# Kernel optimization log

Hardware: AMD Instinct MI355X
Metric: run time of the kernel (lower is better)

The kernel has to match this reference:

```python
import jax, jax.numpy as jnp
import numpy as np

S, B, D_MODEL, H, DH = 2048, 2, 1024, 16, 64
FACTOR = 1.0 / np.sqrt(DH).astype(np.float32)


def setup_inputs() -> dict:
    key = jax.random.key(0)
    ks = jax.random.split(key, 12)
    sc = 0.02
    inp = {
        'query': jax.random.normal(ks[0], (S, B, D_MODEL), jnp.float32),
        'key': jax.random.normal(ks[1], (S, B, D_MODEL), jnp.float32),
        'value': jax.random.normal(ks[2], (S, B, D_MODEL), jnp.float32),
        # causal mask [seq_q, seq_k, 1]; 0 -> masked
        'mask': jnp.tril(jnp.ones((S, S), dtype=bool))[:, :, None],
        'Wq': jax.random.normal(ks[3], (H * DH, D_MODEL), jnp.float32) * sc,
        'bq': jnp.zeros((H * DH,), jnp.float32),
        'Wk': jax.random.normal(ks[4], (H * DH, D_MODEL), jnp.float32) * sc,
        'bk': jnp.zeros((H * DH,), jnp.float32),
        'Wv': jax.random.normal(ks[5], (H * DH, D_MODEL), jnp.float32) * sc,
        'bv': jnp.zeros((H * DH,), jnp.float32),
        'Wo': jax.random.normal(ks[6], (D_MODEL, H * DH), jnp.float32) * sc,
        'bo': jnp.zeros((D_MODEL,), jnp.float32),
    }
    return inp


def _split_heads(x):
    # pattern: 's b (head_dim head_num) -> s b head_num head_dim' (head_dim is OUTER)
    s, b, _ = x.shape
    return x.reshape(s, b, DH, H).transpose(0, 1, 3, 2)  # [s,b,H,DH]


def reference(query, key, value, mask, Wq, bq, Wk, bk, Wv, bv, Wo, bo):
    q = _split_heads(query @ Wq.T + bq)
    k = _split_heads(key @ Wk.T + bk)
    v = _split_heads(value @ Wv.T + bv)
    scores = jnp.einsum('ibhd,jbhd->ijbh', q, k) * FACTOR  # [i,j,b,h]
    scores = jnp.where(mask[..., None], scores, -jnp.inf)
    attn = jax.nn.softmax(scores, axis=1)  # softmax over keys (dim=1)
    out = jnp.einsum('ijbh,jbhd->ibhd', attn, v)  # [i,b,h,d]
    out = out.reshape(S, B, H * DH)  # 'i b h d -> i b (h d)'
    return out @ Wo.T + bo
```

## Files before the change

kernel.cpp:

```cpp
#include <hip/hip_runtime.h>


typedef float f32x4 __attribute__((ext_vector_type(4)));
typedef float f32x16 __attribute__((ext_vector_type(16)));
typedef __bf16 bf16x8_t __attribute__((ext_vector_type(8)));
typedef unsigned short ushort8 __attribute__((ext_vector_type(8)));
typedef unsigned int uint4v __attribute__((ext_vector_type(4)));
typedef unsigned int uint2v __attribute__((ext_vector_type(2)));

#define S_LEN 2048
#define BATCH 2
#define DMODEL 1024
#define NHEAD 16
#define DHEAD 64
#define K_SCALE 0.18033688011112042f

__device__ __forceinline__ unsigned short f2bf(float x) {
  unsigned int u = __builtin_bit_cast(unsigned int, x);
  u += 0x7fffu + ((u >> 16) & 1u);
  return (unsigned short)(u >> 16);
}

__device__ __forceinline__ f32x4 mfma16(ushort8 a, ushort8 b, f32x4 c) {
  return __builtin_amdgcn_mfma_f32_16x16x32_bf16(
      __builtin_bit_cast(bf16x8_t, a), __builtin_bit_cast(bf16x8_t, b), c, 0, 0, 0);
}
__device__ __forceinline__ f32x16 mfma32(ushort8 a, ushort8 b, f32x16 c) {
  return __builtin_amdgcn_mfma_f32_32x32x16_bf16(
      __builtin_bit_cast(bf16x8_t, a), __builtin_bit_cast(bf16x8_t, b), c, 0, 0, 0);
}

__device__ __forceinline__ float max3f(float a, float b, float c) {
  return fmaxf(fmaxf(a, b), c);
}

__device__ __forceinline__ ushort8 pack8(float4 a, float4 b, float s) {
  ushort8 t;
  t[0] = f2bf(a.x * s); t[1] = f2bf(a.y * s); t[2] = f2bf(a.z * s); t[3] = f2bf(a.w * s);
  t[4] = f2bf(b.x * s); t[5] = f2bf(b.y * s); t[6] = f2bf(b.z * s); t[7] = f2bf(b.w * s);
  return t;
}

__device__ __forceinline__ void gload16(unsigned short* lds, const unsigned short* g) {
  __builtin_amdgcn_global_load_lds(
      (const __attribute__((address_space(1))) unsigned int*)g,
      (__attribute__((address_space(3))) unsigned int*)lds, 16, 0, 0);
}

__global__ __launch_bounds__(256) void cvt_kernel(
    const float* __restrict__ q, const float* __restrict__ k, const float* __restrict__ v,
    const float* __restrict__ wq, const float* __restrict__ wk,
    const float* __restrict__ wv, const float* __restrict__ wo,
    unsigned short* __restrict__ qB, unsigned short* __restrict__ kB,
    unsigned short* __restrict__ vB, unsigned short* __restrict__ wqB,
    unsigned short* __restrict__ wkB, unsigned short* __restrict__ wvB,
    unsigned short* __restrict__ woB)
{
  const int c = blockIdx.x * 256 + threadIdx.x;
  const float* s; unsigned short* d; int base;
  if      (c < 524288)  { s = q;  d = qB;  base = 0; }
  else if (c < 1048576) { s = k;  d = kB;  base = 524288; }
  else if (c < 1572864) { s = v;  d = vB;  base = 1048576; }
  else if (c < 1703936) { s = wq; d = wqB; base = 1572864; }
  else if (c < 1835008) { s = wk; d = wkB; base = 1703936; }
  else if (c < 1966080) { s = wv; d = wvB; base = 1835008; }
  else                  { s = wo; d = woB; base = 1966080; }
  const size_t off = (size_t)(c - base) * 8;
  const float4 v0 = *reinterpret_cast<const float4*>(s + off);
  const float4 v1 = *reinterpret_cast<const float4*>(s + off + 4);
  *reinterpret_cast<ushort8*>(d + off) = pack8(v0, v1, 1.0f);
}

__global__ __launch_bounds__(256) void gemm_qkv_kernel(
    const unsigned short* __restrict__ qA, const unsigned short* __restrict__ kA,
    const unsigned short* __restrict__ vA,
    const unsigned short* __restrict__ wqW, const unsigned short* __restrict__ wkW,
    const unsigned short* __restrict__ wvW,
    const float* __restrict__ bq, const float* __restrict__ bk,
    const float* __restrict__ bv,
    unsigned short* __restrict__ Cq, unsigned short* __restrict__ Ck,
    unsigned short* __restrict__ Cv)
{
  __shared__ __align__(16) unsigned short As[2][128 * 64];
  __shared__ __align__(16) unsigned short Ws[2][64 * 64];
  const int z = blockIdx.z;
  const unsigned short* A = (z == 0) ? qA : (z == 1) ? kA : vA;
  const unsigned short* W = (z == 0) ? wqW : (z == 1) ? wkW : wvW;
  const float* bias = (z == 0) ? bq : (z == 1) ? bk : bv;
  unsigned short* C = (z == 0) ? Cq : (z == 1) ? Ck : Cv;
  const float oscale = (z == 1) ? K_SCALE : 1.0f;

  const int tid = threadIdx.x;
  const int lane = tid & 63;
  const int w = tid >> 6;
  const int wm = (w >> 1) * 64, wn = (w & 1) * 32;
  const int g = lane >> 4, lr = lane & 15;

  const int bid = (int)blockIdx.x;
  const int widx = (bid & 7) * 64 + (bid >> 3);
  const int n0 = (widx & 15) * 64;
  const int m0 = (widx >> 4) * 128;

  f32x4 acc[4][2] = {};

#define STAGE(buf, k0)                                                              \
  {                                                                                 \
    _Pragma("unroll")                                                               \
    for (int ii = 0; ii < 4; ++ii) {                                                \
      const int c = ii * 256 + tid;                                                 \
      const int row = c >> 3;                                                       \
      const int sl = (c & 7) ^ (row & 7);                                           \
      gload16(&As[buf][c * 8], A + (size_t)(m0 + row) * DMODEL + (k0) + sl * 8);    \
    }                                                                               \
    _Pragma("unroll")                                                               \
    for (int ii = 0; ii < 2; ++ii) {                                                \
      const int c = ii * 256 + tid;                                                 \
      const int row = c >> 3;                                                       \
      const int sl = (c & 7) ^ (row & 7);                                           \
      gload16(&Ws[buf][c * 8], W + (size_t)(n0 + row) * DMODEL + (k0) + sl * 8);    \
    }                                                                               \
  }

  STAGE(0, 0);
  int cur = 0;

  for (int t = 0; t < 16; ++t) {
    __syncthreads();
    if (t < 15) STAGE(cur ^ 1, (t + 1) * 64);

    const char* ab = (const char*)&As[cur][0];
    const char* wb = (const char*)&Ws[cur][0];
#pragma unroll
    for (int kk = 0; kk < 2; ++kk) {
      ushort8 af[4], bw[2];
#pragma unroll
      for (int mt = 0; mt < 4; ++mt) {
        const int row = wm + mt * 16 + lr;
        af[mt] = *reinterpret_cast<const ushort8*>(
            ab + row * 128 + (((kk * 4 + g) ^ (row & 7)) << 4));
      }
#pragma unroll
      for (int nt = 0; nt < 2; ++nt) {
        const int row = wn + nt * 16 + lr;
        bw[nt] = *reinterpret_cast<const ushort8*>(
            wb + row * 128 + (((kk * 4 + g) ^ (row & 7)) << 4));
      }
      __builtin_amdgcn_s_setprio(1);
#pragma unroll
      for (int mt = 0; mt < 4; ++mt)
#pragma unroll
        for (int nt = 0; nt < 2; ++nt)
          acc[mt][nt] = mfma16(af[mt], bw[nt], acc[mt][nt]);
      __builtin_amdgcn_s_setprio(0);
    }
    cur ^= 1;
  }
#undef STAGE

#pragma unroll
  for (int nt = 0; nt < 2; ++nt) {
    const int col = n0 + wn + nt * 16 + lr;
    const float bvv = bias[col];
#pragma unroll
    for (int mt = 0; mt < 4; ++mt)
#pragma unroll
      for (int r = 0; r < 4; ++r) {
        const int rowg = m0 + wm + mt * 16 + g * 4 + r;
        C[(size_t)rowg * DMODEL + col] = f2bf((acc[mt][nt][r] + bvv) * oscale);
      }
  }
}

__global__ __launch_bounds__(256) void gemm_out_kernel(
    const unsigned short* __restrict__ A, const unsigned short* __restrict__ W,
    const float* __restrict__ bias, float* __restrict__ C)
{
  __shared__ __align__(16) unsigned short As[2][128 * 64];
  __shared__ __align__(16) unsigned short Ws[2][64 * 64];
  const int tid = threadIdx.x;
  const int lane = tid & 63;
  const int w = tid >> 6;
  const int wm = (w >> 1) * 64, wn = (w & 1) * 32;
  const int g = lane >> 4, lr = lane & 15;

  const int bid = (int)blockIdx.x;
  const int widx = (bid & 7) * 64 + (bid >> 3);
  const int n0 = (widx & 15) * 64;
  const int m0 = (widx >> 4) * 128;

  f32x4 acc[4][2] = {};

#define STAGE(buf, k0)                                                              \
  {                                                                                 \
    _Pragma("unroll")                                                               \
    for (int ii = 0; ii < 4; ++ii) {                                                \
      const int c = ii * 256 + tid;                                                 \
      const int row = c >> 3;                                                       \
      const int sl = (c & 7) ^ (row & 7);                                           \
      gload16(&As[buf][c * 8], A + (size_t)(m0 + row) * DMODEL + (k0) + sl * 8);    \
    }                                                                               \
    _Pragma("unroll")                                                               \
    for (int ii = 0; ii < 2; ++ii) {                                                \
      const int c = ii * 256 + tid;                                                 \
      const int row = c >> 3;                                                       \
      const int sl = (c & 7) ^ (row & 7);                                           \
      gload16(&Ws[buf][c * 8], W + (size_t)(n0 + row) * DMODEL + (k0) + sl * 8);    \
    }                                                                               \
  }

  STAGE(0, 0);
  int cur = 0;

  for (int t = 0; t < 16; ++t) {
    __syncthreads();
    if (t < 15) STAGE(cur ^ 1, (t + 1) * 64);

    const char* ab = (const char*)&As[cur][0];
    const char* wb = (const char*)&Ws[cur][0];
#pragma unroll
    for (int kk = 0; kk < 2; ++kk) {
      ushort8 af[4], bw[2];
#pragma unroll
      for (int mt = 0; mt < 4; ++mt) {
        const int row = wm + mt * 16 + lr;
        af[mt] = *reinterpret_cast<const ushort8*>(
            ab + row * 128 + (((kk * 4 + g) ^ (row & 7)) << 4));
      }
#pragma unroll
      for (int nt = 0; nt < 2; ++nt) {
        const int row = wn + nt * 16 + lr;
        bw[nt] = *reinterpret_cast<const ushort8*>(
            wb + row * 128 + (((kk * 4 + g) ^ (row & 7)) << 4));
      }
      __builtin_amdgcn_s_setprio(1);
#pragma unroll
      for (int mt = 0; mt < 4; ++mt)
#pragma unroll
        for (int nt = 0; nt < 2; ++nt)
          acc[mt][nt] = mfma16(af[mt], bw[nt], acc[mt][nt]);
      __builtin_amdgcn_s_setprio(0);
    }
    cur ^= 1;
  }
#undef STAGE

#pragma unroll
  for (int nt = 0; nt < 2; ++nt) {
    const int col = n0 + wn + nt * 16 + lr;
    const float bvv = bias[col];
#pragma unroll
    for (int mt = 0; mt < 4; ++mt)
#pragma unroll
      for (int r = 0; r < 4; ++r) {
        const int rowg = m0 + wm + mt * 16 + g * 4 + r;
        C[(size_t)rowg * DMODEL + col] = acc[mt][nt][r] + bvv;
      }
  }
}

__global__ __launch_bounds__(256) void head_tr0_kernel(
    const unsigned short* __restrict__ in0, unsigned short* __restrict__ out0,
    const unsigned short* __restrict__ in1, unsigned short* __restrict__ out1)
{
  const unsigned short* in = blockIdx.z ? in1 : in0;
  unsigned short* out = blockIdx.z ? out1 : out0;
  __shared__ __align__(16) unsigned short T[32 * 256];
  const int tid = threadIdx.x;
  const int n0 = blockIdx.x * 32, o0 = blockIdx.y * 256;
#pragma unroll
  for (int i = 0; i < 4; ++i) {
    const int c = i * 256 + tid;
    const int row = c >> 5, c8 = c & 31;
    ushort8 v = *reinterpret_cast<const ushort8*>(in + (size_t)(n0 + row) * DMODEL + o0 + c8 * 8);
    int y = (row * 512 + c8 * 16) ^ ((row & 3) << 5);
    *reinterpret_cast<ushort8*>((char*)T + y) = v;
  }
  __syncthreads();
  const int d0 = o0 >> 4, s0 = n0 >> 1;
#pragma unroll
  for (int rep = 0; rep < 2; ++rep) {
    const int e = rep * 256 + tid;
    const int hh = e & 15, s = (e >> 4) & 15, b = (e >> 8) & 1;
    const int n = s * 2 + b;
    unsigned short vals[16];
#pragma unroll
    for (int dd = 0; dd < 16; ++dd) {
      int y = n * 512 + ((dd * 32 + hh * 2) ^ ((n & 3) << 5));
      vals[dd] = *(const unsigned short*)((const char*)T + y);
    }
    uint4v w0, w1;
#pragma unroll
    for (int j = 0; j < 4; ++j) {
      w0[j] = (unsigned)vals[2 * j] | ((unsigned)vals[2 * j + 1] << 16);
      w1[j] = (unsigned)vals[8 + 2 * j] | ((unsigned)vals[8 + 2 * j + 1] << 16);
    }
    unsigned short* dst = out + ((size_t)(b * 16 + hh) * S_LEN + s0 + s) * DHEAD + d0;
    *reinterpret_cast<uint4v*>(dst) = w0;
    *reinterpret_cast<uint4v*>(dst + 8) = w1;
  }
}

__global__ __launch_bounds__(256) void head_tr1_kernel(
    const unsigned short* __restrict__ in, unsigned short* __restrict__ out)
{
  __shared__ __align__(16) unsigned short T[64 * 64];
  const int tid = threadIdx.x;
  const int n0 = blockIdx.x * 64, o0 = blockIdx.y * 64;
#pragma unroll
  for (int i = 0; i < 2; ++i) {
    const int c = i * 256 + tid;
    const int row = c >> 3, c8 = c & 7;
    ushort8 v = *reinterpret_cast<const ushort8*>(in + (size_t)(n0 + row) * DMODEL + o0 + c8 * 8);
    int y = (row * 128 + c8 * 16) ^ ((row & 7) << 4);
    *reinterpret_cast<ushort8*>((char*)T + y) = v;
  }
  __syncthreads();
  const int d0 = o0 >> 4, s0 = n0 >> 1;
  const int shalf = tid & 1, seg = tid >> 1;
  const int dd = seg & 3, hh = (seg >> 2) & 15, b = (seg >> 6) & 1;
  unsigned short vals[16];
#pragma unroll
  for (int i = 0; i < 16; ++i) {
    const int s = shalf * 16 + i;
    const int n = s * 2 + b;
    int y = n * 128 + (((dd * 16 + hh) * 2) ^ ((n & 7) << 4));
    vals[i] = *(const unsigned short*)((const char*)T + y);
  }
  uint4v w0, w1;
#pragma unroll
  for (int j = 0; j < 4; ++j) {
    w0[j] = (unsigned)vals[2 * j] | ((unsigned)vals[2 * j + 1] << 16);
    w1[j] = (unsigned)vals[8 + 2 * j] | ((unsigned)vals[8 + 2 * j + 1] << 16);
  }
  unsigned short* dst = out + ((size_t)(b * 16 + hh) * DHEAD + d0 + dd) * S_LEN + s0 + shalf * 16;
  *reinterpret_cast<uint4v*>(dst) = w0;
  *reinterpret_cast<uint4v*>(dst + 8) = w1;
}

__global__ __launch_bounds__(256, 4) void attn_part_kernel(
    const unsigned short* __restrict__ Qh, const unsigned short* __restrict__ Kh,
    const unsigned short* __restrict__ Vh, unsigned short* __restrict__ Opart,
    float* __restrict__ mlbuf)
{
  __shared__ __align__(16) unsigned short Ks[2][64 * 64];
  __shared__ __align__(16) unsigned short Vs[2][64 * 64];

  const int tid = threadIdx.x;
  const int lane = tid & 63;
  const int w = tid >> 6;
  const int ln31 = lane & 31;
  const int hf = lane >> 5;

  const int u = 39 - (int)blockIdx.x;
  int Q, c;
  if      (u < 4)  { Q = u;                 c = 0; }
  else if (u < 12) { Q = 4 + ((u - 4) >> 1);  c = (u - 4) & 1; }
  else if (u < 24) { Q = 8 + (u - 12) / 3;    c = (u - 12) % 3; }
  else             { Q = 12 + ((u - 24) >> 2); c = (u - 24) & 3; }
  int off;
  if      (Q < 4)  off = Q;
  else if (Q < 8)  off = 4 + (Q - 4) * 2;
  else if (Q < 12) off = 12 + (Q - 8) * 3;
  else             off = 24 + (Q - 12) * 4;

  const int hb = blockIdx.y;
  const int head = hb & 15, b = hb >> 4;
  const int slot = hb * 40 + off + c;
  const int t0 = c * 8;
  const int tmax = 2 * Q + 1;
  const int t1 = (tmax < t0 + 7) ? tmax : (t0 + 7);
  const int q0 = Q * 128;

  const size_t hoff = (size_t)(b * NHEAD + head) * (S_LEN * DHEAD);
  const unsigned short* Qg = Qh + hoff;
  const unsigned short* Kg = Kh + hoff;
  const unsigned short* Vg = Vh + hoff;

  const int qwb = q0 + w * 32;
  const int qg = qwb + ln31;

  ushort8 qf[4];
#pragma unroll
  for (int kt = 0; kt < 4; ++kt)
    qf[kt] = *reinterpret_cast<const ushort8*>(Qg + (size_t)qg * DHEAD + kt * 16 + hf * 8);

  f32x16 oa0 = {0}, oa1 = {0};
  float mrun = -1e30f, ssum = 0.f;

#define STAGE(buf, kv)                                                             \
  {                                                                                \
    _Pragma("unroll")                                                              \
    for (int ii = 0; ii < 2; ++ii) {                                               \
      const int c2 = ii * 256 + tid;                                               \
      const int row = c2 >> 3;                                                     \
      const int sl = (c2 & 7) ^ (row & 7);                                         \
      gload16(&Ks[buf][c2 * 8], Kg + (size_t)((kv) + row) * 64 + sl * 8);          \
    }                                                                              \
    _Pragma("unroll")                                                              \
    for (int ii = 0; ii < 2; ++ii) {                                               \
      const int c2 = ii * 256 + tid;                                               \
      const int row = c2 >> 3;                                                     \
      const int sl = (c2 & 7) ^ (row & 7);                                         \
      gload16(&Vs[buf][c2 * 8], Vg + (size_t)row * S_LEN + (kv) + sl * 8);         \
    }                                                                              \
  }

  STAGE(0, t0 * 64);
  int cur = 0;

  const int kb0 = ln31 * 128 + ((hf * 16) ^ ((ln31 & 7) << 4));
  const int kb1 = (32 + ln31) * 128 + ((hf * 16) ^ ((ln31 & 7) << 4));

  for (int t = t0; t <= t1; ++t) {
    const int kv0 = t * 64;
    __syncthreads();
    if (t < t1) STAGE(cur ^ 1, kv0 + 64);

    if (kv0 <= qwb + 31) {
      f32x16 sc0 = {0}, sc1 = {0};
      {
        const char* ksb = (const char*)&Ks[cur][0];
        __builtin_amdgcn_s_setprio(1);
#pragma unroll
        for (int kt = 0; kt < 4; ++kt) {
          ushort8 kf0 = *reinterpret_cast<const ushort8*>(ksb + (kb0 ^ (kt << 5)));
          ushort8 kf1 = *reinterpret_cast<const ushort8*>(ksb + (kb1 ^ (kt << 5)));
          sc0 = mfma32(kf0, qf[kt], sc0);
          sc1 = mfma32(kf1, qf[kt], sc1);
        }
        __builtin_amdgcn_s_setprio(0);
      }

      if (kv0 + 63 > qwb) {
#pragma unroll
        for (int r = 0; r < 16; ++r) {
          const int keyb = kv0 + (r & 3) + 8 * (r >> 2) + 4 * hf;
          if (keyb > qg) sc0[r] = -1e30f;
          if (keyb + 32 > qg) sc1[r] = -1e30f;
        }
      }

      float m0a = max3f(sc0[0], sc0[1], sc0[2]);
      float m1a = max3f(sc0[3], sc0[4], sc0[5]);
      float m2a = max3f(sc0[6], sc0[7], sc0[8]);
      float m3a = max3f(sc0[9], sc0[10], sc0[11]);
      float m4a = max3f(sc0[12], sc0[13], sc0[14]);
      float m5a = max3f(sc0[15], sc1[0], sc1[1]);
      float m6a = max3f(sc1[2], sc1[3], sc1[4]);
      float m7a = max3f(sc1[5], sc1[6], sc1[7]);
      float m8a = max3f(sc1[8], sc1[9], sc1[10]);
      float m9a = max3f(sc1[11], sc1[12], sc1[13]);
      float mAa = fmaxf(sc1[14], sc1[15]);
      float n0a = max3f(m0a, m1a, m2a);
      float n1a = max3f(m3a, m4a, m5a);
      float n2a = max3f(m6a, m7a, m8a);
      float n3a = fmaxf(m9a, mAa);
      float pmax = fmaxf(max3f(n0a, n1a, n2a), n3a);
      pmax = fmaxf(pmax, __shfl_xor(pmax, 32, 64));

      if (!__all(pmax <= mrun + 8.0f)) {
        const float mnew = fmaxf(mrun, pmax);
        const float scl = exp2f(mrun - mnew);
        ssum *= scl;
#pragma unroll
        for (int r = 0; r < 16; ++r) { oa0[r] *= scl; oa1[r] *= scl; }
        mrun = mnew;
      }

      float pv0[16], pv1[16];
#pragma unroll
      for (int r = 0; r < 16; ++r) {
        pv0[r] = exp2f(sc0[r] - mrun);
        pv1[r] = exp2f(sc1[r] - mrun);
      }
      float a8[8];
#pragma unroll
      for (int r = 0; r < 8; ++r)
        a8[r] = (pv0[r] + pv0[r + 8]) + (pv1[r] + pv1[r + 8]);
      float a4_0 = a8[0] + a8[4], a4_1 = a8[1] + a8[5];
      float a4_2 = a8[2] + a8[6], a4_3 = a8[3] + a8[7];
      float psum = (a4_0 + a4_1) + (a4_2 + a4_3);
      psum += __shfl_xor(psum, 32, 64);
      ssum += psum;

      unsigned int cc[16], pc[16];
#pragma unroll
      for (int j = 0; j < 8; ++j) {
        asm("v_cvt_pk_bf16_f32 %0, %1, %2" : "=v"(cc[j]) : "v"(pv0[2 * j]), "v"(pv0[2 * j + 1]));
        asm("v_cvt_pk_bf16_f32 %0, %1, %2" : "=v"(cc[8 + j]) : "v"(pv1[2 * j]), "v"(pv1[2 * j + 1]));
      }
#pragma unroll
      for (int j = 0; j < 16; ++j)
        pc[j] = (unsigned int)__shfl_xor((int)cc[j], 32, 64);

      uint4v pfw[4];
#pragma unroll
      for (int mt = 0; mt < 2; ++mt) {
#pragma unroll
        for (int ktl = 0; ktl < 2; ++ktl) {
          const int o = mt * 8 + ktl * 4;
          uint4v u4;
          u4[0] = hf ? pc[o + 2] : cc[o + 0];
          u4[1] = hf ? pc[o + 3] : cc[o + 1];
          u4[2] = hf ? cc[o + 2] : pc[o + 0];
          u4[3] = hf ? cc[o + 3] : pc[o + 1];
          pfw[mt * 2 + ktl] = u4;
        }
      }

      {
        const char* vsb = (const char*)&Vs[cur][0];
        __builtin_amdgcn_s_setprio(1);
#pragma unroll
        for (int kt = 0; kt < 4; ++kt) {
          ushort8 vf0 = *reinterpret_cast<const ushort8*>(vsb + (kb0 ^ (kt << 5)));
          ushort8 vf1 = *reinterpret_cast<const ushort8*>(vsb + (kb1 ^ (kt << 5)));
          ushort8 pfr = __builtin_bit_cast(ushort8, pfw[kt]);
          oa0 = mfma32(vf0, pfr, oa0);
          oa1 = mfma32(vf1, pfr, oa1);
        }
        __builtin_amdgcn_s_setprio(0);
      }
    }

    cur ^= 1;
  }
#undef STAGE

  const int ql = w * 32 + ln31;
  unsigned short* ob = Opart + (size_t)slot * 8192 + ql * 64;
#pragma unroll
  for (int mt2 = 0; mt2 < 2; ++mt2) {
#pragma unroll
    for (int rq = 0; rq < 4; ++rq) {
      const int dd = mt2 * 32 + 8 * rq + 4 * hf;
      const f32x16& a = mt2 ? oa1 : oa0;
      unsigned int w0, w1;
      asm("v_cvt_pk_bf16_f32 %0, %1, %2" : "=v"(w0)
          : "v"(a[4 * rq + 0]), "v"(a[4 * rq + 1]));
      asm("v_cvt_pk_bf16_f32 %0, %1, %2" : "=v"(w1)
          : "v"(a[4 * rq + 2]), "v"(a[4 * rq + 3]));
      uint2v pk = { w0, w1 };
      *reinterpret_cast<uint2v*>(ob + dd) = pk;
    }
  }
  if (hf == 0) {
    mlbuf[slot * 256 + ql] = mrun;
    mlbuf[slot * 256 + 128 + ql] = ssum;
  }
}

__global__ __launch_bounds__(256) void attn_combine_kernel(
    const unsigned short* __restrict__ Opart, const float* __restrict__ mlbuf,
    unsigned short* __restrict__ O)
{
  const int Q = blockIdx.x, hb = blockIdx.y;
  const int head = hb & 15, b = hb >> 4;
  const int nch = (2 * Q + 1) / 8 + 1;
  int off;
  if      (Q < 4)  off = Q;
  else if (Q < 8)  off = 4 + (Q - 4) * 2;
  else if (Q < 12) off = 12 + (Q - 8) * 3;
  else             off = 24 + (Q - 12) * 4;
  const int s0 = hb * 40 + off;

  const int tid = threadIdx.x;
  const int q = tid >> 1, dh = (tid & 1) * 32;

  float mc[4], lc[4];
  float M = -1e30f;
  for (int cc = 0; cc < nch; ++cc) {
    mc[cc] = mlbuf[(s0 + cc) * 256 + q];
    lc[cc] = mlbuf[(s0 + cc) * 256 + 128 + q];
    M = fmaxf(M, mc[cc]);
  }
  float L = 0.f, wgt[4];
  for (int cc = 0; cc < nch; ++cc) {
    wgt[cc] = exp2f(mc[cc] - M);
    L += wgt[cc] * lc[cc];
  }
  const float invL = 1.0f / L;

  float acc[32] = {};
  for (int cc = 0; cc < nch; ++cc) {
    const unsigned short* p = Opart + (size_t)(s0 + cc) * 8192 + q * 64 + dh;
    const float wv = wgt[cc];
#pragma unroll
    for (int seg = 0; seg < 4; ++seg) {
      ushort8 v = *reinterpret_cast<const ushort8*>(p + seg * 8);
#pragma unroll
      for (int j = 0; j < 8; ++j) {
        const float f = __builtin_bit_cast(float, ((unsigned int)v[j]) << 16);
        acc[seg * 8 + j] += wv * f;
      }
    }
  }

  unsigned int wpk[16];
#pragma unroll
  for (int j = 0; j < 16; ++j) {
    asm("v_cvt_pk_bf16_f32 %0, %1, %2" : "=v"(wpk[j])
        : "v"(acc[2 * j] * invL), "v"(acc[2 * j + 1] * invL));
  }
  unsigned short* dst = O + ((size_t)((Q * 128 + q) * BATCH + b)) * DMODEL + head * DHEAD + dh;
#pragma unroll
  for (int seg = 0; seg < 4; ++seg)
    *reinterpret_cast<uint4v*>(dst + seg * 8) =
        uint4v{ wpk[4 * seg], wpk[4 * seg + 1], wpk[4 * seg + 2], wpk[4 * seg + 3] };
}

extern "C" void kernel_launch(void* const* d_in, const int* in_sizes, int n_in,
                              void* d_out, int out_size, void* d_ws, size_t ws_size,
                              hipStream_t stream)
{
  (void)in_sizes; (void)n_in; (void)out_size; (void)ws_size;
  const float* query = (const float*)d_in[0];
  const float* key_  = (const float*)d_in[1];
  const float* value = (const float*)d_in[2];
  const float* Wq = (const float*)d_in[4];
  const float* bq = (const float*)d_in[5];
  const float* Wk = (const float*)d_in[6];
  const float* bk = (const float*)d_in[7];
  const float* Wv = (const float*)d_in[8];
  const float* bv = (const float*)d_in[9];
  const float* Wo = (const float*)d_in[10];
  const float* bo = (const float*)d_in[11];
  float* out = (float*)d_out;

  const size_t NE = (size_t)4096 * DMODEL;
  const size_t NW = (size_t)DMODEL * DMODEL;
  unsigned short* qB  = (unsigned short*)d_ws;
  unsigned short* kB  = qB + NE;
  unsigned short* vB  = kB + NE;
  unsigned short* g1  = vB + NE;
  unsigned short* Qh  = g1 + NE;
  unsigned short* Kh  = Qh + NE;
  unsigned short* Vh  = Kh + NE;
  unsigned short* wqB = Vh + NE;
  unsigned short* wkB = wqB + NW;
  unsigned short* wvB = wkB + NW;
  unsigned short* woB = wvB + NW;
  unsigned short* Opart = vB;
  float* mlbuf = (float*)(vB + (size_t)1280 * 8192);

  cvt_kernel<<<dim3(8192), 256, 0, stream>>>(query, key_, value, Wq, Wk, Wv, Wo,
                                             qB, kB, vB, wqB, wkB, wvB, woB);
  gemm_qkv_kernel<<<dim3(512, 1, 3), 256, 0, stream>>>(
      qB, kB, vB, wqB, wkB, wvB, bq, bk, bv, g1, Qh, Kh);
  head_tr0_kernel<<<dim3(128, 4, 2), 256, 0, stream>>>(g1, qB, Qh, Vh);
  head_tr1_kernel<<<dim3(64, 16), 256, 0, stream>>>(Kh, kB);
  attn_part_kernel<<<dim3(40, 32), 256, 0, stream>>>(qB, Vh, kB, Opart, mlbuf);
  attn_combine_kernel<<<dim3(16, 32), 256, 0, stream>>>(Opart, mlbuf, qB);
  gemm_out_kernel<<<dim3(512), 256, 0, stream>>>(qB, woB, bo, out);
}
```

Measured before the change: 141.3 us.

## Merge head transposes into one launch and rebalance attention chunks to six tiles

Combines the two head-transpose kernels into a single launch that dispatches on block index, removing one kernel launch and its tail. The split-KV attention now uses chunks of up to six key tiles (51 chunks per head-batch instead of 40), with a loop-based mapping from block to (query tile, chunk). The combine kernel is adjusted to handle up to six partial chunks. The goal is better load balance and more blocks to fill the GPU, at the cost of more partial outputs to write and merge, and a change in block scheduling order (the old code processed the heaviest query tiles first).

```diff
diff --git a/kernel.cpp b/kernel.cpp
--- a/kernel.cpp
+++ b/kernel.cpp
@@ -14,6 +14,7 @@
 #define NHEAD 16
 #define DHEAD 64
 #define K_SCALE 0.18033688011112042f
+#define NCHUNK 51
 
 __device__ __forceinline__ unsigned short f2bf(float x) {
   unsigned int u = __builtin_bit_cast(unsigned int, x);
@@ -258,35 +259,73 @@
   }
 }
 
-__global__ __launch_bounds__(256) void head_tr0_kernel(
+__global__ __launch_bounds__(256) void transpose_all_kernel(
     const unsigned short* __restrict__ in0, unsigned short* __restrict__ out0,
-    const unsigned short* __restrict__ in1, unsigned short* __restrict__ out1)
+    const unsigned short* __restrict__ in1, unsigned short* __restrict__ out1,
+    const unsigned short* __restrict__ in2, unsigned short* __restrict__ out2)
 {
-  const unsigned short* in = blockIdx.z ? in1 : in0;
-  unsigned short* out = blockIdx.z ? out1 : out0;
   __shared__ __align__(16) unsigned short T[32 * 256];
+  const int bx = (int)blockIdx.x;
   const int tid = threadIdx.x;
-  const int n0 = blockIdx.x * 32, o0 = blockIdx.y * 256;
-#pragma unroll
-  for (int i = 0; i < 4; ++i) {
-    const int c = i * 256 + tid;
-    const int row = c >> 5, c8 = c & 31;
-    ushort8 v = *reinterpret_cast<const ushort8*>(in + (size_t)(n0 + row) * DMODEL + o0 + c8 * 8);
-    int y = (row * 512 + c8 * 16) ^ ((row & 3) << 5);
-    *reinterpret_cast<ushort8*>((char*)T + y) = v;
-  }
-  __syncthreads();
-  const int d0 = o0 >> 4, s0 = n0 >> 1;
-#pragma unroll
-  for (int rep = 0; rep < 2; ++rep) {
-    const int e = rep * 256 + tid;
-    const int hh = e & 15, s = (e >> 4) & 15, b = (e >> 8) & 1;
-    const int n = s * 2 + b;
+
+  if (bx < 1024) {
+    const unsigned short* in = (bx < 512) ? in0 : in1;
+    unsigned short* out = (bx < 512) ? out0 : out1;
+    const int lb = bx & 511;
+    const int n0 = (lb & 127) * 32, o0 = (lb >> 7) * 256;
+#pragma unroll
+    for (int i = 0; i < 4; ++i) {
+      const int c = i * 256 + tid;
+      const int row = c >> 5, c8 = c & 31;
+      ushort8 v = *reinterpret_cast<const ushort8*>(in + (size_t)(n0 + row) * DMODEL + o0 + c8 * 8);
+      int y = (row * 512 + c8 * 16) ^ ((row & 3) << 5);
+      *reinterpret_cast<ushort8*>((char*)T + y) = v;
+    }
+    __syncthreads();
+    const int d0 = o0 >> 4, s0 = n0 >> 1;
+#pragma unroll
+    for (int rep = 0; rep < 2; ++rep) {
+      const int e = rep * 256 + tid;
+      const int hh = e & 15, s = (e >> 4) & 15, b = (e >> 8) & 1;
+      const int n = s * 2 + b;
+      unsigned short vals[16];
+#pragma unroll
+      for (int dd = 0; dd < 16; ++dd) {
+        int y = n * 512 + ((dd * 32 + hh * 2) ^ ((n & 3) << 5));
+        vals[dd] = *(const unsigned short*)((const char*)T + y);
+      }
+      uint4v w0, w1;
+#pragma unroll
+      for (int j = 0; j < 4; ++j) {
+        w0[j] = (unsigned)vals[2 * j] | ((unsigned)vals[2 * j + 1] << 16);
+        w1[j] = (unsigned)vals[8 + 2 * j] | ((unsigned)vals[8 + 2 * j + 1] << 16);
+      }
+      unsigned short* dst = out + ((size_t)(b * 16 + hh) * S_LEN + s0 + s) * DHEAD + d0;
+      *reinterpret_cast<uint4v*>(dst) = w0;
+      *reinterpret_cast<uint4v*>(dst + 8) = w1;
+    }
+  } else {
+    const int lb = bx - 1024;
+    const int n0 = (lb & 63) * 64, o0 = (lb >> 6) * 64;
+#pragma unroll
+    for (int i = 0; i < 2; ++i) {
+      const int c = i * 256 + tid;
+      const int row = c >> 3, c8 = c & 7;
+      ushort8 v = *reinterpret_cast<const ushort8*>(in2 + (size_t)(n0 + row) * DMODEL + o0 + c8 * 8);
+      int y = (row * 128 + c8 * 16) ^ ((row & 7) << 4);
+      *reinterpret_cast<ushort8*>((char*)T + y) = v;
+    }
+    __syncthreads();
+    const int d0 = o0 >> 4, s0 = n0 >> 1;
+    const int shalf = tid & 1, seg = tid >> 1;
+    const int dd = seg & 3, hh = (seg >> 2) & 15, b = (seg >> 6) & 1;
     unsigned short vals[16];
 #pragma unroll
-    for (int dd = 0; dd < 16; ++dd) {
-      int y = n * 512 + ((dd * 32 + hh * 2) ^ ((n & 3) << 5));
-      vals[dd] = *(const unsigned short*)((const char*)T + y);
+    for (int i = 0; i < 16; ++i) {
+      const int s = shalf * 16 + i;
+      const int n = s * 2 + b;
+      int y = n * 128 + (((dd * 16 + hh) * 2) ^ ((n & 7) << 4));
+      vals[i] = *(const unsigned short*)((const char*)T + y);
     }
     uint4v w0, w1;
 #pragma unroll
@@ -294,47 +333,10 @@
       w0[j] = (unsigned)vals[2 * j] | ((unsigned)vals[2 * j + 1] << 16);
       w1[j] = (unsigned)vals[8 + 2 * j] | ((unsigned)vals[8 + 2 * j + 1] << 16);
     }
-    unsigned short* dst = out + ((size_t)(b * 16 + hh) * S_LEN + s0 + s) * DHEAD + d0;
+    unsigned short* dst = out2 + ((size_t)(b * 16 + hh) * DHEAD + d0 + dd) * S_LEN + s0 + shalf * 16;
     *reinterpret_cast<uint4v*>(dst) = w0;
     *reinterpret_cast<uint4v*>(dst + 8) = w1;
   }
-}
-
-__global__ __launch_bounds__(256) void head_tr1_kernel(
-    const unsigned short* __restrict__ in, unsigned short* __restrict__ out)
-{
-  __shared__ __align__(16) unsigned short T[64 * 64];
-  const int tid = threadIdx.x;
-  const int n0 = blockIdx.x * 64, o0 = blockIdx.y * 64;
-#pragma unroll
-  for (int i = 0; i < 2; ++i) {
-    const int c = i * 256 + tid;
-    const int row = c >> 3, c8 = c & 7;
-    ushort8 v = *reinterpret_cast<const ushort8*>(in + (size_t)(n0 + row) * DMODEL + o0 + c8 * 8);
-    int y = (row * 128 + c8 * 16) ^ ((row & 7) << 4);
-    *reinterpret_cast<ushort8*>((char*)T + y) = v;
-  }
-  __syncthreads();
-  const int d0 = o0 >> 4, s0 = n0 >> 1;
-  const int shalf = tid & 1, seg = tid >> 1;
-  const int dd = seg & 3, hh = (seg >> 2) & 15, b = (seg >> 6) & 1;
-  unsigned short vals[16];
-#pragma unroll
-  for (int i = 0; i < 16; ++i) {
-    const int s = shalf * 16 + i;
-    const int n = s * 2 + b;
-    int y = n * 128 + (((dd * 16 + hh) * 2) ^ ((n & 7) << 4));
-    vals[i] = *(const unsigned short*)((const char*)T + y);
-  }
-  uint4v w0, w1;
-#pragma unroll
-  for (int j = 0; j < 4; ++j) {
-    w0[j] = (unsigned)vals[2 * j] | ((unsigned)vals[2 * j + 1] << 16);
-    w1[j] = (unsigned)vals[8 + 2 * j] | ((unsigned)vals[8 + 2 * j + 1] << 16);
-  }
-  unsigned short* dst = out + ((size_t)(b * 16 + hh) * DHEAD + d0 + dd) * S_LEN + s0 + shalf * 16;
-  *reinterpret_cast<uint4v*>(dst) = w0;
-  *reinterpret_cast<uint4v*>(dst + 8) = w1;
 }
 
 __global__ __launch_bounds__(256, 4) void attn_part_kernel(
@@ -351,24 +353,17 @@
   const int ln31 = lane & 31;
   const int hf = lane >> 5;
 
-  const int u = 39 - (int)blockIdx.x;
-  int Q, c;
-  if      (u < 4)  { Q = u;                 c = 0; }
-  else if (u < 12) { Q = 4 + ((u - 4) >> 1);  c = (u - 4) & 1; }
-  else if (u < 24) { Q = 8 + (u - 12) / 3;    c = (u - 12) % 3; }
-  else             { Q = 12 + ((u - 24) >> 2); c = (u - 24) & 3; }
-  int off;
-  if      (Q < 4)  off = Q;
-  else if (Q < 8)  off = 4 + (Q - 4) * 2;
-  else if (Q < 12) off = 12 + (Q - 8) * 3;
-  else             off = 24 + (Q - 12) * 4;
+  int u = (int)blockIdx.x;
+  int Q = 0, nc = 1;
+  while (u >= nc) { u -= nc; ++Q; nc = Q / 3 + 1; }
+  const int c = u;
 
   const int hb = blockIdx.y;
   const int head = hb & 15, b = hb >> 4;
-  const int slot = hb * 40 + off + c;
-  const int t0 = c * 8;
+  const int slot = hb * NCHUNK + (int)blockIdx.x;
+  const int t0 = c * 6;
   const int tmax = 2 * Q + 1;
-  const int t1 = (tmax < t0 + 7) ? tmax : (t0 + 7);
+  const int t1 = (tmax < t0 + 5) ? tmax : (t0 + 5);
   const int q0 = Q * 128;
 
   const size_t hoff = (size_t)(b * NHEAD + head) * (S_LEN * DHEAD);
@@ -556,25 +551,22 @@
 {
   const int Q = blockIdx.x, hb = blockIdx.y;
   const int head = hb & 15, b = hb >> 4;
-  const int nch = (2 * Q + 1) / 8 + 1;
-  int off;
-  if      (Q < 4)  off = Q;
-  else if (Q < 8)  off = 4 + (Q - 4) * 2;
-  else if (Q < 12) off = 12 + (Q - 8) * 3;
-  else             off = 24 + (Q - 12) * 4;
-  const int s0 = hb * 40 + off;
+  const int nch = Q / 3 + 1;
+  int off = 0;
+  for (int j = 0; j < Q; ++j) off += j / 3 + 1;
+  const int s0 = hb * NCHUNK + off;
 
   const int tid = threadIdx.x;
   const int q = tid >> 1, dh = (tid & 1) * 32;
 
-  float mc[4], lc[4];
+  float mc[6], lc[6];
   float M = -1e30f;
   for (int cc = 0; cc < nch; ++cc) {
     mc[cc] = mlbuf[(s0 + cc) * 256 + q];
     lc[cc] = mlbuf[(s0 + cc) * 256 + 128 + q];
     M = fmaxf(M, mc[cc]);
   }
-  float L = 0.f, wgt[4];
+  float L = 0.f, wgt[6];
   for (int cc = 0; cc < nch; ++cc) {
     wgt[cc] = exp2f(mc[cc] - M);
     L += wgt[cc] * lc[cc];
@@ -641,15 +633,14 @@
   unsigned short* wvB = wkB + NW;
   unsigned short* woB = wvB + NW;
   unsigned short* Opart = vB;
-  float* mlbuf = (float*)(vB + (size_t)1280 * 8192);
+  float* mlbuf = (float*)(Opart + (size_t)(NCHUNK * 32) * 8192);
 
   cvt_kernel<<<dim3(8192), 256, 0, stream>>>(query, key_, value, Wq, Wk, Wv, Wo,
                                              qB, kB, vB, wqB, wkB, wvB, woB);
   gemm_qkv_kernel<<<dim3(512, 1, 3), 256, 0, stream>>>(
       qB, kB, vB, wqB, wkB, wvB, bq, bk, bv, g1, Qh, Kh);
-  head_tr0_kernel<<<dim3(128, 4, 2), 256, 0, stream>>>(g1, qB, Qh, Vh);
-  head_tr1_kernel<<<dim3(64, 16), 256, 0, stream>>>(Kh, kB);
-  attn_part_kernel<<<dim3(40, 32), 256, 0, stream>>>(qB, Vh, kB, Opart, mlbuf);
+  transpose_all_kernel<<<dim3(2048), 256, 0, stream>>>(g1, qB, Qh, Vh, Kh, kB);
+  attn_part_kernel<<<dim3(NCHUNK, 32), 256, 0, stream>>>(qB, Vh, kB, Opart, mlbuf);
   attn_combine_kernel<<<dim3(16, 32), 256, 0, stream>>>(Opart, mlbuf, qB);
   gemm_out_kernel<<<dim3(512), 256, 0, stream>>>(qB, woB, bo, out);
 }
```

Result: faster. 137.9 us (-2.4%).
